# Kernel tuning notes

Hardware: AMD Instinct MI355X
Metric: run time of the kernel (lower is better)

## Reference

```python
import jax, jax.numpy as jnp
import numpy as np

U, I, D, B, E = 100000, 50000, 64, 4, 2000000

def setup_inputs() -> dict:
    key = jax.random.key(0)
    k1, k2, k3, k4, k5, k6, k7 = jax.random.split(key, 7)
    user_embedding = jax.random.normal(k1, (U, D), dtype=jnp.float32) * 0.1
    item_embedding = jax.random.normal(k2, (I, D), dtype=jnp.float32) * 0.1
    rows = jax.random.randint(k3, (B, E), 0, U, dtype=jnp.int32)
    cols = jax.random.randint(k4, (B, E), 0, I, dtype=jnp.int32)
    # normalized-adjacency-like small positive values
    vals = jax.random.uniform(k5, (B, E), dtype=jnp.float32) * 0.05
    u_w = jax.random.normal(k6, (D, D), dtype=jnp.float32) * (1.0 / np.sqrt(D))
    i_w = jax.random.normal(k7, (D, D), dtype=jnp.float32) * (1.0 / np.sqrt(D))
    return {"user_embedding": user_embedding, "item_embedding": item_embedding,
            "rows": rows, "cols": cols, "vals": vals, "u_w": u_w, "i_w": i_w}

def reference(user_embedding, item_embedding, rows, cols, vals, u_w, i_w):
    n_users = user_embedding.shape[0]
    n_items = item_embedding.shape[0]

    # per-behavior spmm: A @ item_emb -> [U, D]; AT @ user_emb -> [I, D]
    def spmm_user(r, c, v):
        return jax.ops.segment_sum(v[:, None] * item_embedding[c], r,
                                   num_segments=n_users)

    def spmm_item(r, c, v):
        return jax.ops.segment_sum(v[:, None] * user_embedding[r], c,
                                   num_segments=n_items)

    user_stack = jax.vmap(spmm_user)(rows, cols, vals)  # [B, U, D]
    item_stack = jax.vmap(spmm_item)(rows, cols, vals)  # [B, I, D]

    user_emb = jax.nn.sigmoid(jnp.mean(user_stack, axis=0) @ u_w)   # [U, D]
    item_emb = jax.nn.sigmoid(jnp.mean(item_stack, axis=0) @ i_w)   # [I, D]
    user_embs = jax.nn.sigmoid(jnp.einsum('bud,de->bue', user_stack, u_w))  # [B, U, D]
    item_embs = jax.nn.sigmoid(jnp.einsum('bid,de->bie', item_stack, i_w))  # [B, I, D]
    return user_emb, item_emb, user_embs, item_embs
```

## Files before the change

### kernel.cpp

```cpp
#include <hip/hip_runtime.h>

#define U_N 100000
#define I_N 50000
#define D_N 64
#define B_N 4
#define E_N 2000000

#define EDGES   (B_N * E_N)
#define NSC_U   (U_N / 8)
#define NSC_I   (I_N / 8)
#define CROW    12512
#define NBLK    256
#define EPB     (EDGES / NBLK)
#define CAP     1536
#define SC_T    13


__global__ __launch_bounds__(256) void precompW_kernel(
        const float* __restrict__ emb, const float* __restrict__ W,
        unsigned short* __restrict__ out16, int nrows) {
    __shared__ float Wl[4096];
    __shared__ float xs[4][64];
    int t = threadIdx.x, w = t >> 6, lane = t & 63;
    for (int i = t; i < 4096; i += 256) Wl[i] = W[i];
    int base = blockIdx.x * 32;
#pragma unroll
    for (int it = 0; it < 8; ++it) {
        int row = base + it * 4 + w;
        __syncthreads();
        xs[w][lane] = (row < nrows) ? emb[row * 64 + lane] : 0.f;
        __syncthreads();
        if (row < nrows) {
            float y = 0.f;
#pragma unroll 8
            for (int d = 0; d < 64; ++d)
                y = fmaf(xs[w][d], Wl[d * 64 + lane], y);
            unsigned u = __float_as_uint(y);
            u += 0x7FFFu + ((u >> 16) & 1u);
            out16[row * 64 + lane] = (unsigned short)(u >> 16);
        }
    }
}

__global__ __launch_bounds__(1024) void bhist_kernel(const int* __restrict__ keys,
                                                     unsigned short* __restrict__ cnt16) {
    __shared__ unsigned h[CROW / 2];
    for (int i = threadIdx.x; i < CROW / 2; i += 1024) h[i] = 0;
    __syncthreads();
    int lb = ((blockIdx.x & 7) << 5) | (blockIdx.x >> 3);
    int base = lb * EPB;
    for (int i = threadIdx.x; i < EPB; i += 1024) {
        int rc = keys[base + i] >> 3;
        atomicAdd(&h[rc >> 1], 1u << ((rc & 1) * 16));
    }
    __syncthreads();
    unsigned short* row = cnt16 + (size_t)lb * CROW;
    for (int i = threadIdx.x; i < CROW / 2; i += 1024) {
        unsigned v = h[i];
        row[2 * i]     = (unsigned short)(v & 0xFFFFu);
        row[2 * i + 1] = (unsigned short)(v >> 16);
    }
}

__global__ __launch_bounds__(1024) void scan_tot(const unsigned short* __restrict__ cnt16,
                                                 int nsc, int* __restrict__ cnt_ch) {
    int c = blockIdx.x * 1024 + threadIdx.x;
    if (c >= nsc) return;
    int s = 0;
    for (int lb = 0; lb < NBLK; ++lb) s += cnt16[(size_t)lb * CROW + c];
    cnt_ch[c] = s;
}

__global__ __launch_bounds__(1024) void scan_ex(const int* __restrict__ cnt_ch,
                                                int nsc, int* __restrict__ off_ch) {
    int t = threadIdx.x;
    int loc[SC_T]; int s = 0;
#pragma unroll
    for (int j = 0; j < SC_T; ++j) {
        int idx = t * SC_T + j;
        int c = (idx < nsc) ? cnt_ch[idx] : 0;
        loc[j] = s; s += c;
    }
    __shared__ int sm[1024];
    int mine = s; sm[t] = s; __syncthreads();
    for (int o = 1; o < 1024; o <<= 1) {
        int a = (t >= o) ? sm[t - o] : 0;
        __syncthreads(); sm[t] += a; __syncthreads();
    }
    int pre = sm[t] - mine;
#pragma unroll
    for (int j = 0; j < SC_T; ++j) {
        int idx = t * SC_T + j;
        if (idx < nsc) off_ch[idx] = pre + loc[j];
    }
}

__global__ __launch_bounds__(1024) void scan_cur(const unsigned short* __restrict__ cnt16,
                                                 unsigned short* __restrict__ cur16,
                                                 int nsc) {
    int c = blockIdx.x * 1024 + threadIdx.x;
    if (c >= nsc) return;
    int run = 0;
    for (int lb = 0; lb < NBLK; ++lb) {
        cur16[(size_t)lb * CROW + c] = (unsigned short)run;
        run += cnt16[(size_t)lb * CROW + c];
    }
}

__global__ __launch_bounds__(1024) void cplace_kernel(const int* __restrict__ keys,
                                                      const int* __restrict__ srcs,
                                                      const float* __restrict__ vals,
                                                      const int* __restrict__ off_ch,
                                                      const unsigned short* __restrict__ cur16,
                                                      int nsc,
                                                      uint2* __restrict__ pay) {
    __shared__ int cur[CROW];
    int lb = ((blockIdx.x & 7) << 5) | (blockIdx.x >> 3);
    const unsigned short* crow = cur16 + (size_t)lb * CROW;
    for (int i = threadIdx.x; i < nsc; i += 1024)
        cur[i] = off_ch[i] + (int)crow[i];
    __syncthreads();
    int base = lb * EPB;
    int b = lb >> 6;
    for (int i = threadIdx.x; i < EPB; i += 1024) {
        int gi = base + i;
        int k = keys[gi];
        float v = vals[gi];
        int src = srcs[gi];
        int pos = atomicAdd(&cur[k >> 3], 1);
        pay[pos] = make_uint2(((unsigned)(((k & 7) << 2) | b) << 17) | (unsigned)src,
                              __float_as_uint(v));
    }
}

__global__ __launch_bounds__(512) void fused_kernel(
        const unsigned short* __restrict__ embW16,
        const int* __restrict__ off_ch,
        const int* __restrict__ cnt_ch,
        const uint2* __restrict__ pay,
        float* __restrict__ embs,
        float* __restrict__ mean_out,
        int nrows) {
    int g = blockIdx.x;
    int start = off_ch[g], n = cnt_ch[g];
    int t = threadIdx.x, w = t >> 6, lane = t & 63;

    __shared__ uint2 st2[CAP];
    __shared__ int c32[32];
    __shared__ int bstart[33];
    float* ys = (float*)st2;

    if (n <= CAP) {
        if (t < 32) c32[t] = 0;
        __syncthreads();
        for (int i = t; i < n; i += 512)
            atomicAdd(&c32[pay[start + i].x >> 17], 1);
        __syncthreads();
        if (t == 0) {
            int s = 0;
            for (int b2 = 0; b2 < 32; ++b2) {
                bstart[b2] = s; s += c32[b2]; c32[b2] = bstart[b2];
            }
            bstart[32] = s;
        }
        __syncthreads();
        for (int i = t; i < n; i += 512) {
            uint2 p = pay[start + i];
            int pos = atomicAdd(&c32[p.x >> 17], 1);
            st2[pos] = p;
        }
        __syncthreads();

        int qt = lane >> 4, ql = lane & 15;
        float4 a0, a1, a2, a3;
#define ACC_BIN(AQ, Q)                                                        \
        {                                                                     \
            int s0 = bstart[w * 4 + (Q)], s1 = bstart[w * 4 + (Q) + 1];       \
            AQ = make_float4(0.f, 0.f, 0.f, 0.f);                             \
            for (int j = s0; j < s1; j += 4) {                                \
                int idx = j + qt;                                             \
                int jj = idx < s1 ? idx : s1 - 1;                             \
                uint2 p = st2[jj];                                            \
                float v = (idx < s1) ? __uint_as_float(p.y) : 0.f;            \
                uint2 x = *((const uint2*)(embW16 +                           \
                              (size_t)(p.x & 0x1FFFFu) * 64) + ql);           \
                AQ.x = fmaf(v, __uint_as_float(x.x << 16), AQ.x);             \
                AQ.y = fmaf(v, __uint_as_float(x.x & 0xFFFF0000u), AQ.y);     \
                AQ.z = fmaf(v, __uint_as_float(x.y << 16), AQ.z);             \
                AQ.w = fmaf(v, __uint_as_float(x.y & 0xFFFF0000u), AQ.w);     \
            }                                                                 \
            AQ.x += __shfl_xor(AQ.x, 16); AQ.x += __shfl_xor(AQ.x, 32);       \
            AQ.y += __shfl_xor(AQ.y, 16); AQ.y += __shfl_xor(AQ.y, 32);       \
            AQ.z += __shfl_xor(AQ.z, 16); AQ.z += __shfl_xor(AQ.z, 32);       \
            AQ.w += __shfl_xor(AQ.w, 16); AQ.w += __shfl_xor(AQ.w, 32);       \
        }
        ACC_BIN(a0, 0)
        ACC_BIN(a1, 1)
        ACC_BIN(a2, 2)
        ACC_BIN(a3, 3)
#undef ACC_BIN
        if (qt == 0) {
            int row = g * 8 + w;
            float4 yq[4] = {a0, a1, a2, a3};
#pragma unroll
            for (int q = 0; q < 4; ++q) {
                float4 s4;
                s4.x = 1.f / (1.f + __expf(-yq[q].x));
                s4.y = 1.f / (1.f + __expf(-yq[q].y));
                s4.z = 1.f / (1.f + __expf(-yq[q].z));
                s4.w = 1.f / (1.f + __expf(-yq[q].w));
                *(float4*)&embs[((long long)q * nrows + row) * 64 + 4 * ql] = s4;
            }
            float4 m4;
            m4.x = 0.25f * (a0.x + a1.x + a2.x + a3.x);
            m4.y = 0.25f * (a0.y + a1.y + a2.y + a3.y);
            m4.z = 0.25f * (a0.z + a1.z + a2.z + a3.z);
            m4.w = 0.25f * (a0.w + a1.w + a2.w + a3.w);
            m4.x = 1.f / (1.f + __expf(-m4.x));
            m4.y = 1.f / (1.f + __expf(-m4.y));
            m4.z = 1.f / (1.f + __expf(-m4.z));
            m4.w = 1.f / (1.f + __expf(-m4.w));
            *(float4*)&mean_out[(long long)row * 64 + 4 * ql] = m4;
        }
    } else {
        for (int i = t; i < 2048; i += 512) ys[i] = 0.f;
        __syncthreads();
        for (int j = w; j < n; j += 8) {
            uint2 pv = pay[start + j];
            float x = __uint_as_float(
                (unsigned)embW16[(size_t)(pv.x & 0x1FFFFu) * 64 + lane] << 16);
            atomicAdd(&ys[(pv.x >> 17) * 64 + lane],
                      __uint_as_float(pv.y) * x);
        }
        __syncthreads();
        int row = g * 8 + w;
        float y[4];
#pragma unroll
        for (int q = 0; q < 4; ++q) {
            y[q] = ys[(w * 4 + q) * 64 + lane];
            embs[((long long)q * nrows + row) * 64 + lane] =
                1.f / (1.f + __expf(-y[q]));
        }
        float m = 0.25f * (y[0] + y[1] + y[2] + y[3]);
        mean_out[(long long)row * 64 + lane] = 1.f / (1.f + __expf(-m));
    }
}

__global__ void scatter_atomic_kernel(const float* __restrict__ user_emb,
                                      const float* __restrict__ item_emb,
                                      const int* __restrict__ rows,
                                      const int* __restrict__ cols,
                                      const float* __restrict__ vals,
                                      float* __restrict__ stack_u,
                                      float* __restrict__ stack_i) {
    long long tid = (long long)blockIdx.x * blockDim.x + threadIdx.x;
    long long e  = tid >> 4;
    int lane = (int)(tid & 15);
    if (e >= (long long)EDGES) return;
    int b = (int)(e / E_N);
    int r = rows[e];
    int c = cols[e];
    float v = vals[e];
    const float4* irow = (const float4*)(item_emb + (long long)c * D_N);
    const float4* urow = (const float4*)(user_emb + (long long)r * D_N);
    float4 iv = irow[lane];
    float4 uv = urow[lane];
    float* du = stack_u + ((long long)b * U_N + r) * D_N + lane * 4;
    float* di = stack_i + ((long long)b * I_N + c) * D_N + lane * 4;
    atomicAdd(du + 0, v * iv.x);
    atomicAdd(du + 1, v * iv.y);
    atomicAdd(du + 2, v * iv.z);
    atomicAdd(du + 3, v * iv.w);
    atomicAdd(di + 0, v * uv.x);
    atomicAdd(di + 1, v * uv.y);
    atomicAdd(di + 2, v * uv.z);
    atomicAdd(di + 3, v * uv.w);
}

template <int NROWS>
__global__ __launch_bounds__(64) void transform_kernel(
        float* __restrict__ stack,
        const float* __restrict__ W,
        float* __restrict__ mean_out) {
    const int row = blockIdx.x;
    const int j   = threadIdx.x;
    __shared__ float xs[B_N][D_N];
#pragma unroll
    for (int b = 0; b < B_N; ++b)
        xs[b][j] = stack[((long long)b * NROWS + row) * D_N + j];
    __syncthreads();
    float acc[B_N] = {0.f, 0.f, 0.f, 0.f};
#pragma unroll 8
    for (int d = 0; d < D_N; ++d) {
        float w = W[d * D_N + j];
#pragma unroll
        for (int b = 0; b < B_N; ++b)
            acc[b] += xs[b][d] * w;
    }
    float m = 0.25f * (acc[0] + acc[1] + acc[2] + acc[3]);
#pragma unroll
    for (int b = 0; b < B_N; ++b)
        stack[((long long)b * NROWS + row) * D_N + j] =
            1.0f / (1.0f + __expf(-acc[b]));
    mean_out[(long long)row * D_N + j] = 1.0f / (1.0f + __expf(-m));
}

extern "C" void kernel_launch(void* const* d_in, const int* in_sizes, int n_in,
                              void* d_out, int out_size, void* d_ws, size_t ws_size,
                              hipStream_t stream) {
    const float* user_emb = (const float*)d_in[0];
    const float* item_emb = (const float*)d_in[1];
    const int*   rows     = (const int*)  d_in[2];
    const int*   cols     = (const int*)  d_in[3];
    const float* vals     = (const float*)d_in[4];
    const float* u_w      = (const float*)d_in[5];
    const float* i_w      = (const float*)d_in[6];

    float* out = (float*)d_out;
    float* user_mean = out;
    float* item_mean = out + (long long)U_N * D_N;
    float* stack_u   = item_mean + (long long)I_N * D_N;
    float* stack_i   = stack_u + (long long)B_N * U_N * D_N;

    uint2* pay = (uint2*)d_ws;
    unsigned short* userW16 = (unsigned short*)(pay + EDGES);
    unsigned short* itemW16 = userW16 + (size_t)U_N * D_N;
    unsigned short* cnt16 = itemW16 + (size_t)I_N * D_N;
    unsigned short* cur16 = cnt16 + (size_t)NBLK * CROW;
    int* cnt_ch = (int*)(cur16 + (size_t)NBLK * CROW);
    int* off_ch = cnt_ch + CROW;
    size_t needed = ((char*)(off_ch + CROW)) - (char*)d_ws;

    if (ws_size >= needed) {
        precompW_kernel<<<(I_N + 31) / 32, 256, 0, stream>>>(item_emb, u_w,
                                                             itemW16, I_N);
        precompW_kernel<<<(U_N + 31) / 32, 256, 0, stream>>>(user_emb, i_w,
                                                             userW16, U_N);
        bhist_kernel<<<NBLK, 1024, 0, stream>>>(rows, cnt16);
        scan_tot<<<(NSC_U + 1023) / 1024, 1024, 0, stream>>>(cnt16, NSC_U, cnt_ch);
        scan_ex<<<1, 1024, 0, stream>>>(cnt_ch, NSC_U, off_ch);
        scan_cur<<<(NSC_U + 1023) / 1024, 1024, 0, stream>>>(cnt16, cur16, NSC_U);
        cplace_kernel<<<NBLK, 1024, 0, stream>>>(rows, cols, vals, off_ch, cur16,
                                                 NSC_U, pay);
        fused_kernel<<<NSC_U, 512, 0, stream>>>(itemW16, off_ch, cnt_ch, pay,
                                                stack_u, user_mean, U_N);
        bhist_kernel<<<NBLK, 1024, 0, stream>>>(cols, cnt16);
        scan_tot<<<(NSC_I + 1023) / 1024, 1024, 0, stream>>>(cnt16, NSC_I, cnt_ch);
        scan_ex<<<1, 1024, 0, stream>>>(cnt_ch, NSC_I, off_ch);
        scan_cur<<<(NSC_I + 1023) / 1024, 1024, 0, stream>>>(cnt16, cur16, NSC_I);
        cplace_kernel<<<NBLK, 1024, 0, stream>>>(cols, rows, vals, off_ch, cur16,
                                                 NSC_I, pay);
        fused_kernel<<<NSC_I, 512, 0, stream>>>(userW16, off_ch, cnt_ch, pay,
                                                stack_i, item_mean, I_N);
    } else {
        size_t stack_bytes = sizeof(float) * (size_t)B_N * (U_N + I_N) * D_N;
        hipMemsetAsync(stack_u, 0, stack_bytes, stream);
        long long nthreads = (long long)EDGES * 16;
        int nblocks = (int)((nthreads + 255) / 256);
        scatter_atomic_kernel<<<nblocks, 256, 0, stream>>>(
            user_emb, item_emb, rows, cols, vals, stack_u, stack_i);
        transform_kernel<U_N><<<U_N, 64, 0, stream>>>(stack_u, u_w, user_mean);
        transform_kernel<I_N><<<I_N, 64, 0, stream>>>(stack_i, i_w, item_mean);
    }
}
```

Baseline: 906.1 us.

## Store pre-transformed embeddings in fp32, double histogram blocks, scan counts in place

```diff
diff --git a/kernel.cpp b/kernel.cpp
--- a/kernel.cpp
+++ b/kernel.cpp
@@ -9,8 +9,8 @@
 #define EDGES   (B_N * E_N)
 #define NSC_U   (U_N / 8)
 #define NSC_I   (I_N / 8)
-#define CROW    12512
-#define NBLK    256
+#define CROW    12500
+#define NBLK    512
 #define EPB     (EDGES / NBLK)
 #define CAP     1536
 #define SC_T    13
@@ -18,7 +18,7 @@
 
 __global__ __launch_bounds__(256) void precompW_kernel(
         const float* __restrict__ emb, const float* __restrict__ W,
-        unsigned short* __restrict__ out16, int nrows) {
+        float* __restrict__ outW, int nrows) {
     __shared__ float Wl[4096];
     __shared__ float xs[4][64];
     int t = threadIdx.x, w = t >> 6, lane = t & 63;
@@ -35,9 +35,7 @@
 #pragma unroll 8
             for (int d = 0; d < 64; ++d)
                 y = fmaf(xs[w][d], Wl[d * 64 + lane], y);
-            unsigned u = __float_as_uint(y);
-            u += 0x7FFFu + ((u >> 16) & 1u);
-            out16[row * 64 + lane] = (unsigned short)(u >> 16);
+            outW[row * 64 + lane] = y;
         }
     }
 }
@@ -47,7 +45,7 @@
     __shared__ unsigned h[CROW / 2];
     for (int i = threadIdx.x; i < CROW / 2; i += 1024) h[i] = 0;
     __syncthreads();
-    int lb = ((blockIdx.x & 7) << 5) | (blockIdx.x >> 3);
+    int lb = ((blockIdx.x & 7) << 6) | (blockIdx.x >> 3);
     int base = lb * EPB;
     for (int i = threadIdx.x; i < EPB; i += 1024) {
         int rc = keys[base + i] >> 3;
@@ -95,15 +93,15 @@
     }
 }
 
-__global__ __launch_bounds__(1024) void scan_cur(const unsigned short* __restrict__ cnt16,
-                                                 unsigned short* __restrict__ cur16,
+__global__ __launch_bounds__(1024) void scan_cur(unsigned short* __restrict__ cnt16,
                                                  int nsc) {
     int c = blockIdx.x * 1024 + threadIdx.x;
     if (c >= nsc) return;
     int run = 0;
     for (int lb = 0; lb < NBLK; ++lb) {
-        cur16[(size_t)lb * CROW + c] = (unsigned short)run;
-        run += cnt16[(size_t)lb * CROW + c];
+        int v = cnt16[(size_t)lb * CROW + c];
+        cnt16[(size_t)lb * CROW + c] = (unsigned short)run;
+        run += v;
     }
 }
 
@@ -111,17 +109,17 @@
                                                       const int* __restrict__ srcs,
                                                       const float* __restrict__ vals,
                                                       const int* __restrict__ off_ch,
-                                                      const unsigned short* __restrict__ cur16,
+                                                      const unsigned short* __restrict__ pre16,
                                                       int nsc,
                                                       uint2* __restrict__ pay) {
     __shared__ int cur[CROW];
-    int lb = ((blockIdx.x & 7) << 5) | (blockIdx.x >> 3);
-    const unsigned short* crow = cur16 + (size_t)lb * CROW;
+    int lb = ((blockIdx.x & 7) << 6) | (blockIdx.x >> 3);
+    const unsigned short* crow = pre16 + (size_t)lb * CROW;
     for (int i = threadIdx.x; i < nsc; i += 1024)
         cur[i] = off_ch[i] + (int)crow[i];
     __syncthreads();
     int base = lb * EPB;
-    int b = lb >> 6;
+    int b = lb >> 7;
     for (int i = threadIdx.x; i < EPB; i += 1024) {
         int gi = base + i;
         int k = keys[gi];
@@ -134,7 +132,7 @@
 }
 
 __global__ __launch_bounds__(512) void fused_kernel(
-        const unsigned short* __restrict__ embW16,
+        const float* __restrict__ embW,
         const int* __restrict__ off_ch,
         const int* __restrict__ cnt_ch,
         const uint2* __restrict__ pay,
@@ -182,12 +180,12 @@
                 int jj = idx < s1 ? idx : s1 - 1;                             \
                 uint2 p = st2[jj];                                            \
                 float v = (idx < s1) ? __uint_as_float(p.y) : 0.f;            \
-                uint2 x = *((const uint2*)(embW16 +                           \
+                float4 x = *((const float4*)(embW +                           \
                               (size_t)(p.x & 0x1FFFFu) * 64) + ql);           \
-                AQ.x = fmaf(v, __uint_as_float(x.x << 16), AQ.x);             \
-                AQ.y = fmaf(v, __uint_as_float(x.x & 0xFFFF0000u), AQ.y);     \
-                AQ.z = fmaf(v, __uint_as_float(x.y << 16), AQ.z);             \
-                AQ.w = fmaf(v, __uint_as_float(x.y & 0xFFFF0000u), AQ.w);     \
+                AQ.x = fmaf(v, x.x, AQ.x);                                    \
+                AQ.y = fmaf(v, x.y, AQ.y);                                    \
+                AQ.z = fmaf(v, x.z, AQ.z);                                    \
+                AQ.w = fmaf(v, x.w, AQ.w);                                    \
             }                                                                 \
             AQ.x += __shfl_xor(AQ.x, 16); AQ.x += __shfl_xor(AQ.x, 32);       \
             AQ.y += __shfl_xor(AQ.y, 16); AQ.y += __shfl_xor(AQ.y, 32);       \
@@ -227,8 +225,7 @@
         __syncthreads();
         for (int j = w; j < n; j += 8) {
             uint2 pv = pay[start + j];
-            float x = __uint_as_float(
-                (unsigned)embW16[(size_t)(pv.x & 0x1FFFFu) * 64 + lane] << 16);
+            float x = embW[(size_t)(pv.x & 0x1FFFFu) * 64 + lane];
             atomicAdd(&ys[(pv.x >> 17) * 64 + lane],
                       __uint_as_float(pv.y) * x);
         }
@@ -323,34 +320,33 @@
     float* stack_i   = stack_u + (long long)B_N * U_N * D_N;
 
     uint2* pay = (uint2*)d_ws;
-    unsigned short* userW16 = (unsigned short*)(pay + EDGES);
-    unsigned short* itemW16 = userW16 + (size_t)U_N * D_N;
-    unsigned short* cnt16 = itemW16 + (size_t)I_N * D_N;
-    unsigned short* cur16 = cnt16 + (size_t)NBLK * CROW;
-    int* cnt_ch = (int*)(cur16 + (size_t)NBLK * CROW);
+    float* userWf = (float*)(pay + EDGES);
+    float* itemWf = userWf + (size_t)U_N * D_N;
+    unsigned short* cnt16 = (unsigned short*)(itemWf + (size_t)I_N * D_N);
+    int* cnt_ch = (int*)(cnt16 + (size_t)NBLK * CROW);
     int* off_ch = cnt_ch + CROW;
     size_t needed = ((char*)(off_ch + CROW)) - (char*)d_ws;
 
     if (ws_size >= needed) {
         precompW_kernel<<<(I_N + 31) / 32, 256, 0, stream>>>(item_emb, u_w,
-                                                             itemW16, I_N);
+                                                             itemWf, I_N);
         precompW_kernel<<<(U_N + 31) / 32, 256, 0, stream>>>(user_emb, i_w,
-                                                             userW16, U_N);
+                                                             userWf, U_N);
         bhist_kernel<<<NBLK, 1024, 0, stream>>>(rows, cnt16);
         scan_tot<<<(NSC_U + 1023) / 1024, 1024, 0, stream>>>(cnt16, NSC_U, cnt_ch);
         scan_ex<<<1, 1024, 0, stream>>>(cnt_ch, NSC_U, off_ch);
-        scan_cur<<<(NSC_U + 1023) / 1024, 1024, 0, stream>>>(cnt16, cur16, NSC_U);
-        cplace_kernel<<<NBLK, 1024, 0, stream>>>(rows, cols, vals, off_ch, cur16,
+        scan_cur<<<(NSC_U + 1023) / 1024, 1024, 0, stream>>>(cnt16, NSC_U);
+        cplace_kernel<<<NBLK, 1024, 0, stream>>>(rows, cols, vals, off_ch, cnt16,
                                                  NSC_U, pay);
-        fused_kernel<<<NSC_U, 512, 0, stream>>>(itemW16, off_ch, cnt_ch, pay,
+        fused_kernel<<<NSC_U, 512, 0, stream>>>(itemWf, off_ch, cnt_ch, pay,
                                                 stack_u, user_mean, U_N);
         bhist_kernel<<<NBLK, 1024, 0, stream>>>(cols, cnt16);
         scan_tot<<<(NSC_I + 1023) / 1024, 1024, 0, stream>>>(cnt16, NSC_I, cnt_ch);
         scan_ex<<<1, 1024, 0, stream>>>(cnt_ch, NSC_I, off_ch);
-        scan_cur<<<(NSC_I + 1023) / 1024, 1024, 0, stream>>>(cnt16, cur16, NSC_I);
-        cplace_kernel<<<NBLK, 1024, 0, stream>>>(cols, rows, vals, off_ch, cur16,
+        scan_cur<<<(NSC_I + 1023) / 1024, 1024, 0, stream>>>(cnt16, NSC_I);
+        cplace_kernel<<<NBLK, 1024, 0, stream>>>(cols, rows, vals, off_ch, cnt16,
                                                  NSC_I, pay);
-        fused_kernel<<<NSC_I, 512, 0, stream>>>(userW16, off_ch, cnt_ch, pay,
+        fused_kernel<<<NSC_I, 512, 0, stream>>>(userWf, off_ch, cnt_ch, pay,
                                                 stack_i, item_mean, I_N);
     } else {
         size_t stack_bytes = sizeof(float) * (size_t)B_N * (U_N + I_N) * D_N;
```

After: 1.059 ms. +16.9%, slower.
